# Kernel tuning notes

Hardware: AMD Instinct MI355X
Metric: run time of the kernel (lower is better)

## Reference

```python
import jax, jax.numpy as jnp
import numpy as np

DIM = 768
NUM_HEAD = 12
DIM_HEAD = DIM // NUM_HEAD
SCALE = DIM_HEAD ** -0.5
B, N = 4, 1024


def setup_inputs() -> dict:
    key = jax.random.key(0)
    ks = jax.random.split(key, 6)
    return {
        "x": jax.random.normal(ks[0], (B, N, DIM), jnp.float32),
        "q_weight": jax.random.normal(ks[1], (DIM, DIM), jnp.float32) * 0.02,
        "k_weight": jax.random.normal(ks[2], (DIM, DIM), jnp.float32) * 0.02,
        "v_weight": jax.random.normal(ks[3], (DIM, DIM), jnp.float32) * 0.02,
        "q_bias": jnp.zeros((DIM,), jnp.float32),
        "k_bias": jnp.zeros((DIM,), jnp.float32),
        "v_bias": jnp.zeros((DIM,), jnp.float32),
        "proj_weight": jax.random.normal(ks[4], (DIM, DIM), jnp.float32) * 0.02,
        "proj_bias": jax.random.normal(ks[5], (DIM,), jnp.float32) * 0.02,
    }


def reference(x, q_weight, k_weight, v_weight, q_bias, k_bias, v_bias,
              proj_weight, proj_bias):
    B_, N_, C = x.shape
    shortcut = x
    # pre-norm: torch .std() is unbiased (ddof=1)
    mean = jnp.mean(x, axis=-1, keepdims=True)
    std = jnp.std(x, axis=-1, keepdims=True, ddof=1)
    xn = (x - mean) / std
    # F.linear: x @ W.T + b
    q = xn @ q_weight.T + q_bias
    k = xn @ k_weight.T + k_bias
    v = xn @ v_weight.T + v_bias
    # b n (h d) -> b h n d
    q = q.reshape(B_, N_, NUM_HEAD, DIM_HEAD).transpose(0, 2, 1, 3)
    k = k.reshape(B_, N_, NUM_HEAD, DIM_HEAD).transpose(0, 2, 1, 3)
    v = v.reshape(B_, N_, NUM_HEAD, DIM_HEAD).transpose(0, 2, 1, 3)
    attn = jnp.einsum('bhqd,bhkd->bhqk', q, k * SCALE)
    attn = jax.nn.softmax(attn, axis=-1)
    out = jnp.einsum('bhqk,bhkd->bhqd', attn, v)
    out = out.transpose(0, 2, 1, 3).reshape(B_, N_, C)
    out = out @ proj_weight.T + proj_bias
    return out + shortcut
```

## Files before the change

### kernel.cpp

```cpp
#include <hip/hip_runtime.h>

typedef unsigned short ushort_t;
typedef unsigned int uint_t;
typedef __attribute__((ext_vector_type(8))) unsigned short ushort8;
typedef __attribute__((ext_vector_type(2))) unsigned int uint2v;
typedef __attribute__((ext_vector_type(8))) __bf16 bf16x8;
typedef __attribute__((ext_vector_type(4))) float floatx4;

#define DIM 768
#define NHEAD 12
#define DHEAD 64
#define SEQ 1024
#define BATCH 4
#define TOKENS (BATCH * SEQ)
#define WELEM (DIM * DIM)
#define SCALE_LOG2E 0.18033688011112042f

static __device__ __forceinline__ uint_t fbits(float f) {
  union { float f; uint_t u; } c; c.f = f; return c.u;
}
static __device__ __forceinline__ ushort_t f2bf(float f) {
  return (ushort_t)((fbits(f) + 0x8000u) >> 16);
}
static __device__ __forceinline__ uint_t pack_bf2(float lo, float hi) {
  const uint_t a = fbits(lo) + 0x8000u, b = fbits(hi) + 0x8000u;
#if __has_builtin(__builtin_amdgcn_perm)
  return __builtin_amdgcn_perm(b, a, 0x07060302u);
#else
  return (a >> 16) | (b & 0xFFFF0000u);
#endif
}
static __device__ __forceinline__ float fexp2(float x) {
#if __has_builtin(__builtin_amdgcn_exp2f)
  return __builtin_amdgcn_exp2f(x);
#else
  return exp2f(x);
#endif
}
static __device__ __forceinline__ floatx4 mfma16(ushort8 a, ushort8 b, floatx4 c) {
  return __builtin_amdgcn_mfma_f32_16x16x32_bf16(
      __builtin_bit_cast(bf16x8, a), __builtin_bit_cast(bf16x8, b), c, 0, 0, 0);
}
static __device__ __forceinline__ void gload_lds16(const ushort_t* g,
                                                   ushort_t* l) {
  __builtin_amdgcn_global_load_lds(
      (const __attribute__((address_space(1))) void*)g,
      (__attribute__((address_space(3))) void*)l, 16, 0, 0);
}

__global__ __launch_bounds__(256) void cvt_kernel(
    const float* __restrict__ qw, const float* __restrict__ kw,
    const float* __restrict__ vw, const float* __restrict__ pw,
    ushort_t* __restrict__ dst) {
  const float* s = (blockIdx.y == 0) ? qw : (blockIdx.y == 1) ? kw
                  : (blockIdx.y == 2) ? vw : pw;
  ushort_t* d = dst + (size_t)blockIdx.y * WELEM;
  const int i = (blockIdx.x * 256 + threadIdx.x) * 4;
  const float4 f = *(const float4*)&s[i];
  uint2v o;
  o[0] = pack_bf2(f.x, f.y);
  o[1] = pack_bf2(f.z, f.w);
  *(uint2v*)&d[i] = o;
}

__global__ __launch_bounds__(256) void ln_kernel(const float* __restrict__ x,
                                                 ushort_t* __restrict__ xn) {
  const int wave = threadIdx.x >> 6, lane = threadIdx.x & 63;
  const int row = blockIdx.x * 4 + wave;
  const float4* xr = (const float4*)(x + (size_t)row * DIM);
  float4 v[3];
  float s = 0.f, s2 = 0.f;
#pragma unroll
  for (int j = 0; j < 3; ++j) {
    v[j] = xr[j * 64 + lane];
    s += v[j].x + v[j].y + v[j].z + v[j].w;
    s2 += v[j].x * v[j].x + v[j].y * v[j].y + v[j].z * v[j].z + v[j].w * v[j].w;
  }
#pragma unroll
  for (int off = 1; off < 64; off <<= 1) {
    s += __shfl_xor(s, off);
    s2 += __shfl_xor(s2, off);
  }
  const float mean = s * (1.f / 768.f);
  const float var = (s2 - 768.f * mean * mean) * (1.f / 767.f);
  const float rstd = rsqrtf(var);
  ushort_t* xo = xn + (size_t)row * DIM;
#pragma unroll
  for (int j = 0; j < 3; ++j) {
    uint2v o;
    o[0] = pack_bf2((v[j].x - mean) * rstd, (v[j].y - mean) * rstd);
    o[1] = pack_bf2((v[j].z - mean) * rstd, (v[j].w - mean) * rstd);
    *(uint2v*)&xo[(j * 64 + lane) * 4] = o;
  }
}

#define BK 64
__global__ __launch_bounds__(256) void qkv_kernel(
    const ushort_t* __restrict__ xn, const ushort_t* __restrict__ wbf,
    const float* __restrict__ qb, const float* __restrict__ kb,
    const float* __restrict__ vb,
    ushort_t* __restrict__ qh, ushort_t* __restrict__ kh,
    ushort_t* __restrict__ vt) {
  __shared__ ushort_t As[128 * BK];
  __shared__ ushort_t Bs[128 * BK];
  const int tid = threadIdx.x;
  const int wave = tid >> 6, lane = tid & 63, quad = lane >> 4, l15 = lane & 15;
  const int m0 = blockIdx.x * 128;
  const int mat = blockIdx.y / 6, nb = blockIdx.y % 6;
  const int n0 = nb * 128;
  const ushort_t* W = wbf + (size_t)mat * WELEM;
  const int chan_off = (wave >> 1) * 64, tok_off = (wave & 1) * 64;
  const int srow8 = lane >> 3;
  const int schunk = (lane & 7) ^ srow8;
  const int l7 = l15 & 7;

  floatx4 acc[4][4];
#pragma unroll
  for (int i = 0; i < 4; ++i)
#pragma unroll
    for (int j = 0; j < 4; ++j) acc[i][j] = (floatx4){0.f, 0.f, 0.f, 0.f};

  for (int k0 = 0; k0 < DIM; k0 += BK) {
#pragma unroll
    for (int i = 0; i < 4; ++i) {
      const int c = wave * 4 + i;
      const int row = c * 8 + srow8;
      gload_lds16(&xn[(size_t)(m0 + row) * DIM + k0 + schunk * 8], &As[c * 512]);
      gload_lds16(&W[(size_t)(n0 + row) * DIM + k0 + schunk * 8], &Bs[c * 512]);
    }
    __syncthreads();
    ushort8 af[4][2], bfr[4][2];
#pragma unroll
    for (int i = 0; i < 4; ++i)
#pragma unroll
      for (int k2 = 0; k2 < 2; ++k2) {
        const int ch = ((k2 * 4 + quad) ^ l7) * 8;
        bfr[i][k2] = *(const ushort8*)&Bs[(chan_off + i * 16 + l15) * BK + ch];
        af[i][k2] = *(const ushort8*)&As[(tok_off + i * 16 + l15) * BK + ch];
      }
#pragma unroll
    for (int k2 = 0; k2 < 2; ++k2)
#pragma unroll
      for (int i = 0; i < 4; ++i)
#pragma unroll
        for (int j = 0; j < 4; ++j)
          acc[i][j] = mfma16(bfr[i][k2], af[j][k2], acc[i][j]);
    __syncthreads();
  }

  if (mat != 2) {
    const float* bias = (mat == 0) ? qb : kb;
    ushort_t* dst = (mat == 0) ? qh : kh;
    const float os = (mat == 0) ? SCALE_LOG2E : 1.0f;
    const int hh = (n0 + chan_off) >> 6;
#pragma unroll
    for (int i = 0; i < 4; ++i) {
      const int ch0 = n0 + chan_off + i * 16 + quad * 4;
      const float4 bv = *(const float4*)&bias[ch0];
      const int d0 = i * 16 + quad * 4;
#pragma unroll
      for (int j = 0; j < 4; ++j) {
        const int tok = m0 + tok_off + j * 16 + l15;
        const int bb = tok >> 10, nn = tok & 1023;
        uint2v pk;
        pk[0] = pack_bf2((acc[i][j][0] + bv.x) * os, (acc[i][j][1] + bv.y) * os);
        pk[1] = pack_bf2((acc[i][j][2] + bv.z) * os, (acc[i][j][3] + bv.w) * os);
        *(uint2v*)&dst[(size_t)((bb * NHEAD + hh) * SEQ + nn) * DHEAD + d0] = pk;
      }
    }
  } else {
#pragma unroll
    for (int i = 0; i < 4; ++i) {
      const int ch0 = n0 + chan_off + i * 16 + quad * 4;
      const float4 bv = *(const float4*)&vb[ch0];
      const float bvf[4] = {bv.x, bv.y, bv.z, bv.w};
      const int hh = ch0 >> 6, d0 = ch0 & 63;
#pragma unroll
      for (int j = 0; j < 4; ++j) {
        const int tok = m0 + tok_off + j * 16 + l15;
        const int bb = tok >> 10, nn = tok & 1023;
        const int t2 = (nn >> 4) & 3;
        const int goff = (nn & ~63) + l15 * 4 + t2;
        const size_t base = (size_t)((bb * NHEAD + hh) * DHEAD + d0) * SEQ;
#pragma unroll
        for (int r = 0; r < 4; ++r)
          vt[base + (size_t)r * SEQ + goff] = f2bf(acc[i][j][r] + bvf[r]);
      }
    }
  }
}

#define PSTR 68
__global__ __launch_bounds__(256) void attn_kernel(
    const ushort_t* __restrict__ qh, const ushort_t* __restrict__ kh,
    const ushort_t* __restrict__ vt, ushort_t* __restrict__ ao) {
  __shared__ ushort_t kv[2][2][4096];
  __shared__ ushort_t Ps[4][16 * PSTR];
  float* cb = (float*)&kv[0][0][0];
  const int tid = threadIdx.x;
  const int wave = tid >> 6, lane = tid & 63, quad = lane >> 4, l15 = lane & 15;
  const int l7 = l15 & 7;
  const int grp = wave >> 1, wsub = wave & 1;
  const int h = blockIdx.y, b = blockIdx.z;
  const int basekv = ((b * NHEAD + h) * SEQ) * DHEAD;
  const int basevt = ((b * NHEAD + h) * DHEAD) * SEQ;
  const int q0 = blockIdx.x * 64 + wsub * 32;
  const int kbase = grp * 512;

  ushort8 qf[2][2];
#pragma unroll
  for (int w = 0; w < 2; ++w) {
    const ushort_t* Qr = qh + basekv + (q0 + w * 16 + l15) * DHEAD;
    qf[w][0] = *(const ushort8*)&Qr[quad * 8];
    qf[w][1] = *(const ushort8*)&Qr[32 + quad * 8];
  }
  ushort8 ones;
#pragma unroll
  for (int i = 0; i < 8; ++i) ones[i] = 0x3F80;

  floatx4 o[2][4];
#pragma unroll
  for (int w = 0; w < 2; ++w)
#pragma unroll
    for (int t = 0; t < 4; ++t) o[w][t] = (floatx4){0.f, 0.f, 0.f, 0.f};
  floatx4 acc_l[2] = {(floatx4){0.f, 0.f, 0.f, 0.f},
                      (floatx4){0.f, 0.f, 0.f, 0.f}};

  const int srow8 = lane >> 3, schunk = (lane & 7) ^ srow8;

  for (int kt = 0; kt < 512; kt += 64) {
#pragma unroll
    for (int i = 0; i < 4; ++i) {
      const int c = wsub * 4 + i;
      gload_lds16(&kh[basekv + (kbase + kt + c * 8 + srow8) * DHEAD + schunk * 8],
                  &kv[grp][0][c * 512]);
      gload_lds16(&vt[basevt + (c * 8 + srow8) * SEQ + kbase + kt + schunk * 8],
                  &kv[grp][1][c * 512]);
    }
    __syncthreads();

    floatx4 sacc[2][4];
#pragma unroll
    for (int w = 0; w < 2; ++w)
#pragma unroll
      for (int s = 0; s < 4; ++s) sacc[w][s] = (floatx4){0.f, 0.f, 0.f, 0.f};
#pragma unroll
    for (int s = 0; s < 4; ++s) {
#pragma unroll
      for (int hh = 0; hh < 2; ++hh) {
        const ushort8 kf = *(const ushort8*)&kv[grp][0][(s * 16 + l15) * 64 +
                                                        (((hh * 4 + quad) ^ l7) * 8)];
#pragma unroll
        for (int w = 0; w < 2; ++w)
          sacc[w][s] = mfma16(qf[w][hh], kf, sacc[w][s]);
      }
    }

#pragma unroll
    for (int w = 0; w < 2; ++w) {
#pragma unroll
      for (int r = 0; r < 4; ++r) {
        uint2v pk;
        pk[0] = pack_bf2(fexp2(sacc[w][0][r]), fexp2(sacc[w][1][r]));
        pk[1] = pack_bf2(fexp2(sacc[w][2][r]), fexp2(sacc[w][3][r]));
        *(uint2v*)&Ps[wave][(quad * 4 + r) * PSTR + l15 * 4] = pk;
      }
    }

#pragma unroll
    for (int hh = 0; hh < 2; ++hh) {
      ushort8 pf[2];
#pragma unroll
      for (int w = 0; w < 2; ++w) {
        pf[w] = *(const ushort8*)&Ps[wave][l15 * PSTR + hh * 32 + quad * 8];
        acc_l[w] = mfma16(pf[w], ones, acc_l[w]);
      }
#pragma unroll
      for (int t = 0; t < 4; ++t) {
        const ushort8 vf = *(const ushort8*)&kv[grp][1][(t * 16 + l15) * 64 +
                                                        (((hh * 4 + quad) ^ l7) * 8)];
#pragma unroll
        for (int w = 0; w < 2; ++w) o[w][t] = mfma16(pf[w], vf, o[w][t]);
      }
    }
    __syncthreads();
  }

  const int cb0 = wsub * (32 * 66);
  if (grp == 1) {
#pragma unroll
    for (int w = 0; w < 2; ++w) {
#pragma unroll
      for (int t = 0; t < 4; ++t)
#pragma unroll
        for (int r = 0; r < 4; ++r)
          cb[cb0 + (w * 16 + quad * 4 + r) * 66 + t * 16 + l15] = o[w][t][r];
      if (l15 == 0)
#pragma unroll
        for (int r = 0; r < 4; ++r)
          cb[cb0 + (w * 16 + quad * 4 + r) * 66 + 64] = acc_l[w][r];
    }
  }
  __syncthreads();
  if (grp == 0) {
#pragma unroll
    for (int w = 0; w < 2; ++w) {
#pragma unroll
      for (int r = 0; r < 4; ++r) {
        const int row = w * 16 + quad * 4 + r;
        const float l = acc_l[w][r] + cb[cb0 + row * 66 + 64];
        const float rl = 1.f / l;
        const int token = b * SEQ + q0 + row;
#pragma unroll
        for (int t = 0; t < 4; ++t) {
          const float val = o[w][t][r] + cb[cb0 + row * 66 + t * 16 + l15];
          ao[(size_t)token * DIM + h * DHEAD + t * 16 + l15] = f2bf(val * rl);
        }
      }
    }
  }
}

__global__ __launch_bounds__(256) void proj_kernel(
    const ushort_t* __restrict__ ao, const ushort_t* __restrict__ pwb,
    const float* __restrict__ pb, const float* __restrict__ x,
    float* __restrict__ out) {
  __shared__ ushort_t As[64 * BK];
  __shared__ ushort_t Bs[128 * BK];
  const int tid = threadIdx.x;
  const int wave = tid >> 6, lane = tid & 63, quad = lane >> 4, l15 = lane & 15;
  const int m0 = blockIdx.x * 64;
  const int n0 = blockIdx.y * 128;
  const int chan_off = (wave >> 1) * 64, tok_off = (wave & 1) * 32;
  const int srow8 = lane >> 3;
  const int schunk = (lane & 7) ^ srow8;
  const int l7 = l15 & 7;

  floatx4 acc[4][2];
#pragma unroll
  for (int i = 0; i < 4; ++i)
#pragma unroll
    for (int j = 0; j < 2; ++j) acc[i][j] = (floatx4){0.f, 0.f, 0.f, 0.f};

  for (int k0 = 0; k0 < DIM; k0 += BK) {
#pragma unroll
    for (int i = 0; i < 2; ++i) {
      const int c = wave * 2 + i;
      const int row = c * 8 + srow8;
      gload_lds16(&ao[(size_t)(m0 + row) * DIM + k0 + schunk * 8], &As[c * 512]);
    }
#pragma unroll
    for (int i = 0; i < 4; ++i) {
      const int c = wave * 4 + i;
      const int row = c * 8 + srow8;
      gload_lds16(&pwb[(size_t)(n0 + row) * DIM + k0 + schunk * 8], &Bs[c * 512]);
    }
    __syncthreads();
    ushort8 af[2][2], bfr[4][2];
#pragma unroll
    for (int k2 = 0; k2 < 2; ++k2) {
      const int ch = ((k2 * 4 + quad) ^ l7) * 8;
#pragma unroll
      for (int j = 0; j < 2; ++j)
        af[j][k2] = *(const ushort8*)&As[(tok_off + j * 16 + l15) * BK + ch];
#pragma unroll
      for (int i = 0; i < 4; ++i)
        bfr[i][k2] = *(const ushort8*)&Bs[(chan_off + i * 16 + l15) * BK + ch];
    }
#pragma unroll
    for (int k2 = 0; k2 < 2; ++k2)
#pragma unroll
      for (int i = 0; i < 4; ++i)
#pragma unroll
        for (int j = 0; j < 2; ++j)
          acc[i][j] = mfma16(bfr[i][k2], af[j][k2], acc[i][j]);
    __syncthreads();
  }

#pragma unroll
  for (int i = 0; i < 4; ++i) {
    const int ch0 = n0 + chan_off + i * 16 + quad * 4;
    const float4 bv = *(const float4*)&pb[ch0];
#pragma unroll
    for (int j = 0; j < 2; ++j) {
      const int tok = m0 + tok_off + j * 16 + l15;
      const float4 res = *(const float4*)&x[(size_t)tok * DIM + ch0];
      float4 ov;
      ov.x = acc[i][j][0] + bv.x + res.x;
      ov.y = acc[i][j][1] + bv.y + res.y;
      ov.z = acc[i][j][2] + bv.z + res.z;
      ov.w = acc[i][j][3] + bv.w + res.w;
      *(float4*)&out[(size_t)tok * DIM + ch0] = ov;
    }
  }
}

extern "C" void kernel_launch(void* const* d_in, const int* in_sizes, int n_in,
                              void* d_out, int out_size, void* d_ws,
                              size_t ws_size, hipStream_t stream) {
  const float* x  = (const float*)d_in[0];
  const float* qw = (const float*)d_in[1];
  const float* kw = (const float*)d_in[2];
  const float* vw = (const float*)d_in[3];
  const float* qb = (const float*)d_in[4];
  const float* kb = (const float*)d_in[5];
  const float* vb = (const float*)d_in[6];
  const float* pw = (const float*)d_in[7];
  const float* pb = (const float*)d_in[8];
  float* out = (float*)d_out;

  ushort_t* ws = (ushort_t*)d_ws;
  const size_t NTOK = (size_t)TOKENS * DIM;
  ushort_t* xn  = ws;
  ushort_t* qh  = ws + NTOK;
  ushort_t* kh  = ws + 2 * NTOK;
  ushort_t* vt  = ws + 3 * NTOK;
  ushort_t* wbf = ws + 4 * NTOK;
  ushort_t* ao  = xn;

  cvt_kernel<<<dim3(WELEM / 1024, 4), 256, 0, stream>>>(qw, kw, vw, pw, wbf);
  ln_kernel<<<TOKENS / 4, 256, 0, stream>>>(x, xn);
  qkv_kernel<<<dim3(32, 18), 256, 0, stream>>>(xn, wbf, qb, kb, vb, qh, kh, vt);
  attn_kernel<<<dim3(16, NHEAD, BATCH), 256, 0, stream>>>(qh, kh, vt, ao);
  proj_kernel<<<dim3(64, 6), 256, 0, stream>>>(ao, wbf + 3 * (size_t)WELEM, pb,
                                               x, out);
}
```

Baseline: 159.4 us.

## Restructure attention into per-wave double-buffered 32-key tiles without block syncs

The attention kernel moves from 4 waves that split the key range in two and merge partial sums through LDS, to 2 waves per block. Each wave walks all 1024 keys in 32-key tiles and double-buffers its own K/V tiles in LDS, waiting on vmcnt instead of __syncthreads. The V-transpose layout written by the QKV kernel is changed to match the 32-key tile interleave. This removes block-wide barriers and the cross-group reduction epilogue and overlaps loads with compute. In exchange there are fewer waves per block, smaller MFMA batches per tile, and correctness now depends on per-wave waitcnt ordering.

```diff
diff --git a/kernel.cpp b/kernel.cpp
--- a/kernel.cpp
+++ b/kernel.cpp
@@ -179,8 +179,8 @@
       for (int j = 0; j < 4; ++j) {
         const int tok = m0 + tok_off + j * 16 + l15;
         const int bb = tok >> 10, nn = tok & 1023;
-        const int t2 = (nn >> 4) & 3;
-        const int goff = (nn & ~63) + l15 * 4 + t2;
+        const int t2 = (nn >> 4) & 1;
+        const int goff = (nn & ~31) + l15 * 2 + t2;
         const size_t base = (size_t)((bb * NHEAD + hh) * DHEAD + d0) * SEQ;
 #pragma unroll
         for (int r = 0; r < 4; ++r)
@@ -190,22 +190,19 @@
   }
 }
 
-#define PSTR 68
-__global__ __launch_bounds__(256) void attn_kernel(
+#define PSTR2 34
+__global__ __launch_bounds__(128) void attn_kernel(
     const ushort_t* __restrict__ qh, const ushort_t* __restrict__ kh,
     const ushort_t* __restrict__ vt, ushort_t* __restrict__ ao) {
-  __shared__ ushort_t kv[2][2][4096];
-  __shared__ ushort_t Ps[4][16 * PSTR];
-  float* cb = (float*)&kv[0][0][0];
+  __shared__ ushort_t kv[2][2][2][2048];
+  __shared__ ushort_t Ps[2][2][16 * PSTR2];
   const int tid = threadIdx.x;
   const int wave = tid >> 6, lane = tid & 63, quad = lane >> 4, l15 = lane & 15;
   const int l7 = l15 & 7;
-  const int grp = wave >> 1, wsub = wave & 1;
   const int h = blockIdx.y, b = blockIdx.z;
   const int basekv = ((b * NHEAD + h) * SEQ) * DHEAD;
   const int basevt = ((b * NHEAD + h) * DHEAD) * SEQ;
-  const int q0 = blockIdx.x * 64 + wsub * 32;
-  const int kbase = grp * 512;
+  const int q0 = blockIdx.x * 64 + wave * 32;
 
   ushort8 qf[2][2];
 #pragma unroll
@@ -226,30 +223,45 @@
   floatx4 acc_l[2] = {(floatx4){0.f, 0.f, 0.f, 0.f},
                       (floatx4){0.f, 0.f, 0.f, 0.f}};
 
-  const int srow8 = lane >> 3, schunk = (lane & 7) ^ srow8;
-
-  for (int kt = 0; kt < 512; kt += 64) {
-#pragma unroll
-    for (int i = 0; i < 4; ++i) {
-      const int c = wsub * 4 + i;
-      gload_lds16(&kh[basekv + (kbase + kt + c * 8 + srow8) * DHEAD + schunk * 8],
-                  &kv[grp][0][c * 512]);
-      gload_lds16(&vt[basevt + (c * 8 + srow8) * SEQ + kbase + kt + schunk * 8],
-                  &kv[grp][1][c * 512]);
-    }
-    __syncthreads();
-
-    floatx4 sacc[2][4];
+  const int ksrow = lane >> 3;
+  const int kschunk = (lane & 7) ^ ksrow;
+  const int vdrow = lane >> 2;
+  const int vchunk = (lane & 3) ^ (vdrow & 3);
+
+  auto prefetch = [&](int kt, int buf) {
+#pragma unroll
+    for (int c = 0; c < 4; ++c)
+      gload_lds16(&kh[basekv + (kt + c * 8 + ksrow) * DHEAD + kschunk * 8],
+                  &kv[wave][buf][0][c * 512]);
+#pragma unroll
+    for (int c = 0; c < 4; ++c)
+      gload_lds16(&vt[basevt + (c * 16 + vdrow) * SEQ + kt + vchunk * 8],
+                  &kv[wave][buf][1][c * 512]);
+  };
+
+  prefetch(0, 0);
+  int buf = 0;
+  for (int kt = 0; kt < SEQ; kt += 32) {
+    if (kt + 32 < SEQ) {
+      prefetch(kt + 32, buf ^ 1);
+      __builtin_amdgcn_s_waitcnt(0x0F78);
+    } else {
+      __builtin_amdgcn_s_waitcnt(0x0F70);
+    }
+    const ushort_t* K = &kv[wave][buf][0][0];
+    const ushort_t* V = &kv[wave][buf][1][0];
+
+    floatx4 sacc[2][2];
 #pragma unroll
     for (int w = 0; w < 2; ++w)
 #pragma unroll
-      for (int s = 0; s < 4; ++s) sacc[w][s] = (floatx4){0.f, 0.f, 0.f, 0.f};
-#pragma unroll
-    for (int s = 0; s < 4; ++s) {
+      for (int s = 0; s < 2; ++s) sacc[w][s] = (floatx4){0.f, 0.f, 0.f, 0.f};
+#pragma unroll
+    for (int s = 0; s < 2; ++s) {
 #pragma unroll
       for (int hh = 0; hh < 2; ++hh) {
-        const ushort8 kf = *(const ushort8*)&kv[grp][0][(s * 16 + l15) * 64 +
-                                                        (((hh * 4 + quad) ^ l7) * 8)];
+        const ushort8 kf = *(const ushort8*)&K[(s * 16 + l15) * 64 +
+                                               (((hh * 4 + quad) ^ l7) * 8)];
 #pragma unroll
         for (int w = 0; w < 2; ++w)
           sacc[w][s] = mfma16(qf[w][hh], kf, sacc[w][s]);
@@ -257,68 +269,40 @@
     }
 
 #pragma unroll
+    for (int w = 0; w < 2; ++w)
+#pragma unroll
+      for (int r = 0; r < 4; ++r) {
+        const uint_t pk = pack_bf2(fexp2(sacc[w][0][r]), fexp2(sacc[w][1][r]));
+        *(uint_t*)&Ps[wave][w][(quad * 4 + r) * PSTR2 + l15 * 2] = pk;
+      }
+
+    ushort8 pf[2];
+#pragma unroll
     for (int w = 0; w < 2; ++w) {
-#pragma unroll
-      for (int r = 0; r < 4; ++r) {
-        uint2v pk;
-        pk[0] = pack_bf2(fexp2(sacc[w][0][r]), fexp2(sacc[w][1][r]));
-        pk[1] = pack_bf2(fexp2(sacc[w][2][r]), fexp2(sacc[w][3][r]));
-        *(uint2v*)&Ps[wave][(quad * 4 + r) * PSTR + l15 * 4] = pk;
-      }
-    }
-
-#pragma unroll
-    for (int hh = 0; hh < 2; ++hh) {
-      ushort8 pf[2];
-#pragma unroll
-      for (int w = 0; w < 2; ++w) {
-        pf[w] = *(const ushort8*)&Ps[wave][l15 * PSTR + hh * 32 + quad * 8];
-        acc_l[w] = mfma16(pf[w], ones, acc_l[w]);
-      }
-#pragma unroll
-      for (int t = 0; t < 4; ++t) {
-        const ushort8 vf = *(const ushort8*)&kv[grp][1][(t * 16 + l15) * 64 +
-                                                        (((hh * 4 + quad) ^ l7) * 8)];
-#pragma unroll
-        for (int w = 0; w < 2; ++w) o[w][t] = mfma16(pf[w], vf, o[w][t]);
-      }
-    }
-    __syncthreads();
-  }
-
-  const int cb0 = wsub * (32 * 66);
-  if (grp == 1) {
-#pragma unroll
-    for (int w = 0; w < 2; ++w) {
+      pf[w] = *(const ushort8*)&Ps[wave][w][l15 * PSTR2 + quad * 8];
+      acc_l[w] = mfma16(pf[w], ones, acc_l[w]);
+    }
+#pragma unroll
+    for (int t = 0; t < 4; ++t) {
+      const ushort8 vf = *(const ushort8*)&V[(t * 16 + l15) * 32 +
+                                             ((quad ^ (l15 & 3)) * 8)];
+#pragma unroll
+      for (int w = 0; w < 2; ++w) o[w][t] = mfma16(pf[w], vf, o[w][t]);
+    }
+    buf ^= 1;
+  }
+
+#pragma unroll
+  for (int w = 0; w < 2; ++w)
+#pragma unroll
+    for (int r = 0; r < 4; ++r) {
+      const float rl = 1.f / acc_l[w][r];
+      const int token = b * SEQ + q0 + w * 16 + quad * 4 + r;
 #pragma unroll
       for (int t = 0; t < 4; ++t)
-#pragma unroll
-        for (int r = 0; r < 4; ++r)
-          cb[cb0 + (w * 16 + quad * 4 + r) * 66 + t * 16 + l15] = o[w][t][r];
-      if (l15 == 0)
-#pragma unroll
-        for (int r = 0; r < 4; ++r)
-          cb[cb0 + (w * 16 + quad * 4 + r) * 66 + 64] = acc_l[w][r];
-    }
-  }
-  __syncthreads();
-  if (grp == 0) {
-#pragma unroll
-    for (int w = 0; w < 2; ++w) {
-#pragma unroll
-      for (int r = 0; r < 4; ++r) {
-        const int row = w * 16 + quad * 4 + r;
-        const float l = acc_l[w][r] + cb[cb0 + row * 66 + 64];
-        const float rl = 1.f / l;
-        const int token = b * SEQ + q0 + row;
-#pragma unroll
-        for (int t = 0; t < 4; ++t) {
-          const float val = o[w][t][r] + cb[cb0 + row * 66 + t * 16 + l15];
-          ao[(size_t)token * DIM + h * DHEAD + t * 16 + l15] = f2bf(val * rl);
-        }
-      }
-    }
-  }
+        ao[(size_t)token * DIM + h * DHEAD + t * 16 + l15] =
+            f2bf(o[w][t][r] * rl);
+    }
 }
 
 __global__ __launch_bounds__(256) void proj_kernel(
@@ -421,7 +405,7 @@
   cvt_kernel<<<dim3(WELEM / 1024, 4), 256, 0, stream>>>(qw, kw, vw, pw, wbf);
   ln_kernel<<<TOKENS / 4, 256, 0, stream>>>(x, xn);
   qkv_kernel<<<dim3(32, 18), 256, 0, stream>>>(xn, wbf, qb, kb, vb, qh, kh, vt);
-  attn_kernel<<<dim3(16, NHEAD, BATCH), 256, 0, stream>>>(qh, kh, vt, ao);
+  attn_kernel<<<dim3(16, NHEAD, BATCH), 128, 0, stream>>>(qh, kh, vt, ao);
   proj_kernel<<<dim3(64, 6), 256, 0, stream>>>(ao, wbf + 3 * (size_t)WELEM, pb,
                                                x, out);
 }
```

New measurement: 172.7 us. +8.3%, slower.

## Double-buffer LDS tiles in QKV and proj GEMMs; merge weight-convert and layernorm

Applied to the files above, without the earlier changes.

Both the QKV and output-projection GEMMs now keep two LDS buffers and issue the global-to-LDS loads for the next K tile before computing on the current one. This drops one barrier per iteration and hides global load latency behind the MFMA work. Separately, the weight bf16 conversion and the layernorm are merged into one launch, so one kernel launch and one inter-kernel gap go away. Doubling LDS use may reduce occupancy. Correctness depends on the async LDS loads having completed by the single barrier.

```diff
diff --git a/kernel.cpp b/kernel.cpp
--- a/kernel.cpp
+++ b/kernel.cpp
@@ -48,61 +48,64 @@
       (__attribute__((address_space(3))) void*)l, 16, 0, 0);
 }
 
-__global__ __launch_bounds__(256) void cvt_kernel(
+__global__ __launch_bounds__(256) void prep_kernel(
     const float* __restrict__ qw, const float* __restrict__ kw,
     const float* __restrict__ vw, const float* __restrict__ pw,
-    ushort_t* __restrict__ dst) {
-  const float* s = (blockIdx.y == 0) ? qw : (blockIdx.y == 1) ? kw
-                  : (blockIdx.y == 2) ? vw : pw;
-  ushort_t* d = dst + (size_t)blockIdx.y * WELEM;
-  const int i = (blockIdx.x * 256 + threadIdx.x) * 4;
-  const float4 f = *(const float4*)&s[i];
-  uint2v o;
-  o[0] = pack_bf2(f.x, f.y);
-  o[1] = pack_bf2(f.z, f.w);
-  *(uint2v*)&d[i] = o;
-}
-
-__global__ __launch_bounds__(256) void ln_kernel(const float* __restrict__ x,
-                                                 ushort_t* __restrict__ xn) {
-  const int wave = threadIdx.x >> 6, lane = threadIdx.x & 63;
-  const int row = blockIdx.x * 4 + wave;
-  const float4* xr = (const float4*)(x + (size_t)row * DIM);
-  float4 v[3];
-  float s = 0.f, s2 = 0.f;
-#pragma unroll
-  for (int j = 0; j < 3; ++j) {
-    v[j] = xr[j * 64 + lane];
-    s += v[j].x + v[j].y + v[j].z + v[j].w;
-    s2 += v[j].x * v[j].x + v[j].y * v[j].y + v[j].z * v[j].z + v[j].w * v[j].w;
-  }
-#pragma unroll
-  for (int off = 1; off < 64; off <<= 1) {
-    s += __shfl_xor(s, off);
-    s2 += __shfl_xor(s2, off);
-  }
-  const float mean = s * (1.f / 768.f);
-  const float var = (s2 - 768.f * mean * mean) * (1.f / 767.f);
-  const float rstd = rsqrtf(var);
-  ushort_t* xo = xn + (size_t)row * DIM;
-#pragma unroll
-  for (int j = 0; j < 3; ++j) {
+    const float* __restrict__ x, ushort_t* __restrict__ wbf,
+    ushort_t* __restrict__ xn) {
+  const int bid = blockIdx.x;
+  if (bid < 2304) {
+    const int mat = bid / 576, inner = bid % 576;
+    const float* s = (mat == 0) ? qw : (mat == 1) ? kw : (mat == 2) ? vw : pw;
+    ushort_t* d = wbf + (size_t)mat * WELEM;
+    const int i = (inner * 256 + threadIdx.x) * 4;
+    const float4 f = *(const float4*)&s[i];
     uint2v o;
-    o[0] = pack_bf2((v[j].x - mean) * rstd, (v[j].y - mean) * rstd);
-    o[1] = pack_bf2((v[j].z - mean) * rstd, (v[j].w - mean) * rstd);
-    *(uint2v*)&xo[(j * 64 + lane) * 4] = o;
+    o[0] = pack_bf2(f.x, f.y);
+    o[1] = pack_bf2(f.z, f.w);
+    *(uint2v*)&d[i] = o;
+  } else {
+    const int wave = threadIdx.x >> 6, lane = threadIdx.x & 63;
+    const int row = (bid - 2304) * 4 + wave;
+    const float4* xr = (const float4*)(x + (size_t)row * DIM);
+    float4 v[3];
+    float s = 0.f, s2 = 0.f;
+#pragma unroll
+    for (int j = 0; j < 3; ++j) {
+      v[j] = xr[j * 64 + lane];
+      s += v[j].x + v[j].y + v[j].z + v[j].w;
+      s2 += v[j].x * v[j].x + v[j].y * v[j].y + v[j].z * v[j].z +
+            v[j].w * v[j].w;
+    }
+#pragma unroll
+    for (int off = 1; off < 64; off <<= 1) {
+      s += __shfl_xor(s, off);
+      s2 += __shfl_xor(s2, off);
+    }
+    const float mean = s * (1.f / 768.f);
+    const float var = (s2 - 768.f * mean * mean) * (1.f / 767.f);
+    const float rstd = rsqrtf(var);
+    ushort_t* xo = xn + (size_t)row * DIM;
+#pragma unroll
+    for (int j = 0; j < 3; ++j) {
+      uint2v o;
+      o[0] = pack_bf2((v[j].x - mean) * rstd, (v[j].y - mean) * rstd);
+      o[1] = pack_bf2((v[j].z - mean) * rstd, (v[j].w - mean) * rstd);
+      *(uint2v*)&xo[(j * 64 + lane) * 4] = o;
+    }
   }
 }
 
 #define BK 64
+#define NKIT (DIM / BK)
 __global__ __launch_bounds__(256) void qkv_kernel(
     const ushort_t* __restrict__ xn, const ushort_t* __restrict__ wbf,
     const float* __restrict__ qb, const float* __restrict__ kb,
     const float* __restrict__ vb,
     ushort_t* __restrict__ qh, ushort_t* __restrict__ kh,
     ushort_t* __restrict__ vt) {
-  __shared__ ushort_t As[128 * BK];
-  __shared__ ushort_t Bs[128 * BK];
+  __shared__ ushort_t As[2][128 * BK];
+  __shared__ ushort_t Bs[2][128 * BK];
   const int tid = threadIdx.x;
   const int wave = tid >> 6, lane = tid & 63, quad = lane >> 4, l15 = lane & 15;
   const int m0 = blockIdx.x * 128;
@@ -120,23 +123,31 @@
 #pragma unroll
     for (int j = 0; j < 4; ++j) acc[i][j] = (floatx4){0.f, 0.f, 0.f, 0.f};
 
-  for (int k0 = 0; k0 < DIM; k0 += BK) {
+  auto stage = [&](int k0, int bf) {
 #pragma unroll
     for (int i = 0; i < 4; ++i) {
       const int c = wave * 4 + i;
       const int row = c * 8 + srow8;
-      gload_lds16(&xn[(size_t)(m0 + row) * DIM + k0 + schunk * 8], &As[c * 512]);
-      gload_lds16(&W[(size_t)(n0 + row) * DIM + k0 + schunk * 8], &Bs[c * 512]);
-    }
+      gload_lds16(&xn[(size_t)(m0 + row) * DIM + k0 + schunk * 8],
+                  &As[bf][c * 512]);
+      gload_lds16(&W[(size_t)(n0 + row) * DIM + k0 + schunk * 8],
+                  &Bs[bf][c * 512]);
+    }
+  };
+
+  stage(0, 0);
+  for (int it = 0; it < NKIT; ++it) {
+    const int cur = it & 1;
     __syncthreads();
+    if (it + 1 < NKIT) stage((it + 1) * BK, cur ^ 1);
     ushort8 af[4][2], bfr[4][2];
 #pragma unroll
     for (int i = 0; i < 4; ++i)
 #pragma unroll
       for (int k2 = 0; k2 < 2; ++k2) {
         const int ch = ((k2 * 4 + quad) ^ l7) * 8;
-        bfr[i][k2] = *(const ushort8*)&Bs[(chan_off + i * 16 + l15) * BK + ch];
-        af[i][k2] = *(const ushort8*)&As[(tok_off + i * 16 + l15) * BK + ch];
+        bfr[i][k2] = *(const ushort8*)&Bs[cur][(chan_off + i * 16 + l15) * BK + ch];
+        af[i][k2] = *(const ushort8*)&As[cur][(tok_off + i * 16 + l15) * BK + ch];
       }
 #pragma unroll
     for (int k2 = 0; k2 < 2; ++k2)
@@ -145,7 +156,6 @@
 #pragma unroll
         for (int j = 0; j < 4; ++j)
           acc[i][j] = mfma16(bfr[i][k2], af[j][k2], acc[i][j]);
-    __syncthreads();
   }
 
   if (mat != 2) {
@@ -325,8 +335,8 @@
     const ushort_t* __restrict__ ao, const ushort_t* __restrict__ pwb,
     const float* __restrict__ pb, const float* __restrict__ x,
     float* __restrict__ out) {
-  __shared__ ushort_t As[64 * BK];
-  __shared__ ushort_t Bs[128 * BK];
+  __shared__ ushort_t As[2][64 * BK];
+  __shared__ ushort_t Bs[2][128 * BK];
   const int tid = threadIdx.x;
   const int wave = tid >> 6, lane = tid & 63, quad = lane >> 4, l15 = lane & 15;
   const int m0 = blockIdx.x * 64;
@@ -342,30 +352,38 @@
 #pragma unroll
     for (int j = 0; j < 2; ++j) acc[i][j] = (floatx4){0.f, 0.f, 0.f, 0.f};
 
-  for (int k0 = 0; k0 < DIM; k0 += BK) {
+  auto stage = [&](int k0, int bf) {
 #pragma unroll
     for (int i = 0; i < 2; ++i) {
       const int c = wave * 2 + i;
       const int row = c * 8 + srow8;
-      gload_lds16(&ao[(size_t)(m0 + row) * DIM + k0 + schunk * 8], &As[c * 512]);
+      gload_lds16(&ao[(size_t)(m0 + row) * DIM + k0 + schunk * 8],
+                  &As[bf][c * 512]);
     }
 #pragma unroll
     for (int i = 0; i < 4; ++i) {
       const int c = wave * 4 + i;
       const int row = c * 8 + srow8;
-      gload_lds16(&pwb[(size_t)(n0 + row) * DIM + k0 + schunk * 8], &Bs[c * 512]);
-    }
+      gload_lds16(&pwb[(size_t)(n0 + row) * DIM + k0 + schunk * 8],
+                  &Bs[bf][c * 512]);
+    }
+  };
+
+  stage(0, 0);
+  for (int it = 0; it < NKIT; ++it) {
+    const int cur = it & 1;
     __syncthreads();
+    if (it + 1 < NKIT) stage((it + 1) * BK, cur ^ 1);
     ushort8 af[2][2], bfr[4][2];
 #pragma unroll
     for (int k2 = 0; k2 < 2; ++k2) {
       const int ch = ((k2 * 4 + quad) ^ l7) * 8;
 #pragma unroll
       for (int j = 0; j < 2; ++j)
-        af[j][k2] = *(const ushort8*)&As[(tok_off + j * 16 + l15) * BK + ch];
+        af[j][k2] = *(const ushort8*)&As[cur][(tok_off + j * 16 + l15) * BK + ch];
 #pragma unroll
       for (int i = 0; i < 4; ++i)
-        bfr[i][k2] = *(const ushort8*)&Bs[(chan_off + i * 16 + l15) * BK + ch];
+        bfr[i][k2] = *(const ushort8*)&Bs[cur][(chan_off + i * 16 + l15) * BK + ch];
     }
 #pragma unroll
     for (int k2 = 0; k2 < 2; ++k2)
@@ -374,7 +392,6 @@
 #pragma unroll
         for (int j = 0; j < 2; ++j)
           acc[i][j] = mfma16(bfr[i][k2], af[j][k2], acc[i][j]);
-    __syncthreads();
   }
 
 #pragma unroll
@@ -418,8 +435,7 @@
   ushort_t* wbf = ws + 4 * NTOK;
   ushort_t* ao  = xn;
 
-  cvt_kernel<<<dim3(WELEM / 1024, 4), 256, 0, stream>>>(qw, kw, vw, pw, wbf);
-  ln_kernel<<<TOKENS / 4, 256, 0, stream>>>(x, xn);
+  prep_kernel<<<2304 + TOKENS / 4, 256, 0, stream>>>(qw, kw, vw, pw, x, wbf, xn);
   qkv_kernel<<<dim3(32, 18), 256, 0, stream>>>(xn, wbf, qb, kb, vb, qh, kh, vt);
   attn_kernel<<<dim3(16, NHEAD, BATCH), 256, 0, stream>>>(qh, kh, vt, ao);
   proj_kernel<<<dim3(64, 6), 256, 0, stream>>>(ao, wbf + 3 * (size_t)WELEM, pb,
```

Measured after the change: 156.8 us. About the same (-1.6%).
